# Performance work log

Hardware: AMD Instinct MI355X
Metric: run time of the kernel (lower is better)

Reference implementation:

```python
import jax, jax.numpy as jnp
import numpy as np
from jax import lax

BS, K, N = 8, 8, 16            # batch, gathers per sample, picks per curve
T, WG = 3072, 64               # gather time samples, traces
H, WC = 256, 256               # CVEncoder ScaleSize
RH, RW = 1024, 512             # resize (also GatherEncoder outLen=RH)
T0, T1 = 0.0, 7000.0           # tInt[0], tInt[-1]


def setup_inputs() -> dict:
    key = jax.random.key(0)
    ks = jax.random.split(key, 8)
    gather = jax.random.normal(ks[0], (BS, K, T, WG), jnp.float32)
    # cv: times sorted, strictly > 0, within [T0, T1]; velocities within VMM range
    times = jnp.sort(jax.random.uniform(ks[1], (BS, K, N), minval=100.0, maxval=T1), axis=-1)
    vels = jnp.sort(jax.random.uniform(ks[2], (BS, K, N), minval=1500.0, maxval=4500.0), axis=-1)
    cv = jnp.stack([times, vels], axis=-1).astype(jnp.float32)
    VMM = jnp.tile(jnp.array([1500.0, 4500.0], jnp.float32), (BS, 1))
    def cw(k, shape):
        return (jax.random.normal(k, shape, jnp.float32) * 0.1)
    params = dict(
        w1=cw(ks[3], (1, 1, 3, 3)), b1=jnp.zeros((1,), jnp.float32), g1=jnp.ones((1,), jnp.float32), be1=jnp.zeros((1,), jnp.float32),
        w2=cw(ks[4], (2, 3, 3, 3)), b2=jnp.zeros((2,), jnp.float32), g2=jnp.ones((2,), jnp.float32), be2=jnp.zeros((2,), jnp.float32),
        w3=cw(ks[5], (1, 2, 3, 2)), b3=jnp.zeros((1,), jnp.float32), g3=jnp.ones((1,), jnp.float32), be3=jnp.zeros((1,), jnp.float32),
        wf=cw(ks[6], (1, 1, 3, 3)), bf=jnp.zeros((1,), jnp.float32), gf=jnp.ones((1,), jnp.float32), bef=jnp.zeros((1,), jnp.float32),
    )
    return {"gather": gather, "cv": cv, "VMM": VMM, **params}


def _conv(x, w, b, stride, pad):
    y = lax.conv_general_dilated(x, w, stride, pad, dimension_numbers=("NCHW", "OIHW", "NCHW"))
    return y + b[None, :, None, None]


def _bn(x, g, b, eps=1e-5):
    # training-mode BatchNorm2d: stats over (N, H, W)
    m = jnp.mean(x, (0, 2, 3), keepdims=True)
    v = jnp.var(x, (0, 2, 3), keepdims=True)
    return (x - m) / jnp.sqrt(v + eps) * g[None, :, None, None] + b[None, :, None, None]


def _lrelu(x):
    return jnp.where(x >= 0, x, 0.1 * x)


def _cbl(x, w, b, g, be, stride):
    return _lrelu(_bn(_conv(x, w, b, stride, "VALID"), g, be))


def _maxpool(x, k):
    p = k // 2
    return lax.reduce_window(x, -jnp.inf, lax.max, (1, 1, k, k), (1, 1, 1, 1),
                             ((0, 0), (0, 0), (p, p), (p, p)))


def _cv_mask(cv, VMM):
    # normalize times to fractional row index and velocities to fractional col index
    dt = (T1 - T0) / (H - 1)
    t_idx = (cv[..., 0] - T0) / dt                                        # (BS,K,N)
    dv = (VMM[:, 1] - VMM[:, 0]) / (WC - 1)                               # (BS,)
    v_idx = (cv[..., 1] - VMM[:, 0, None, None]) / dv[:, None, None]      # (BS,K,N)
    t_flat = t_idx.reshape(-1, N)
    v_flat = v_idx.reshape(-1, N)
    tq = jnp.arange(H, dtype=jnp.float32)
    # per-curve piecewise-linear interpolation of v over the time grid
    v_curve = jax.vmap(lambda xp, fp: jnp.interp(tq, xp, fp))(t_flat, v_flat)  # (M,H)
    v_int = jnp.clip(v_curve.astype(jnp.int32), 0, WC - 1)
    M = BS * K
    mask = jnp.full((M, H, WC), 0.01, jnp.float32)
    mask = mask.at[jnp.arange(M)[:, None], jnp.arange(H)[None, :], v_int].add(0.9)
    mask = mask.reshape(BS, K, H, WC)
    # bilinear resize, half-pixel centers == torch align_corners=False
    return jax.image.resize(mask, (BS, K, RH, RW), method="linear")


def _forward(gather, cv, VMM, w1, b1, g1, be1, w2, b2, g2, be2, w3, b3, g3, be3, wf, bf, gf, bef):
    cv_mask = lax.stop_gradient(_cv_mask(cv, VMM))          # CVEncoder runs under no_grad
    x = gather.reshape(-1, 1, T, WG)                        # (BS*K,1,T,WG)
    x = x / jnp.max(jnp.abs(x))                             # mode='mute': keep sign
    x = _cbl(x, w1, b1, g1, be1, (3, 2))                    # (M,1,1024,31)
    xcat = jnp.concatenate([x, _maxpool(x, 3), _maxpool(x, 5)], axis=1)
    x = _cbl(xcat, w2, b2, g2, be2, (3, 2))                 # (M,2,341,15)
    x = _cbl(x, w3, b3, g3, be3, (3, 2))                    # (M,1,113,7)
    x = jax.image.resize(x, (x.shape[0], 1, RH, 1), method="linear")
    genr = x.reshape(BS, K, RH, 1)
    mix = jnp.sum(genr * cv_mask, axis=1, keepdims=True)    # (BS,1,RH,RW)
    y = _conv(mix, wf, bf, (1, 1), ((1, 1), (1, 1)))
    return _lrelu(_bn(y, gf, bef))


def reference(gather, cv, VMM, w1, b1, g1, be1, w2, b2, g2, be2, w3, b3, g3, be3, wf, bf, gf, bef):
    return _forward(gather, cv, VMM, w1, b1, g1, be1, w2, b2, g2, be2, w3, b3, g3, be3, wf, bf, gf, bef)
```

## Files before the change

### kernel.cpp

```cpp
#include <hip/hip_runtime.h>
#include <math.h>

#define BSZ 8
#define KG  8
#define NP  16
#define MM  64
#define TT  3072
#define WGN 64
#define HH  256
#define WCN 256
#define RHN 1024
#define RWN 512

#define C1H 1024
#define C1W 31
#define C2H 341
#define C2W 15
#define C3H 113
#define C3W 7

#define N1 (MM*C1H*C1W)
#define N2 (MM*C2H*C2W)
#define N3 (MM*C3H*C3W)
#define NF (BSZ*RHN*RWN)

#define SL 8

#define OFF_VINT 768
#define OFF_Y1   (OFF_VINT + MM*HH*4)
#define OFF_Y2   (OFF_Y1  + N1*4)
#define OFF_Y3   (OFF_Y2  + 2*N2*4)
#define OFF_GENR (OFF_Y3  + N3*4)

__device__ __forceinline__ void blockAdd2(double s, double ss, double* o0, double* o1) {
    __shared__ double red[4][2];
    __syncthreads();
    int lane = threadIdx.x & 63, wid = threadIdx.x >> 6;
#pragma unroll
    for (int off = 32; off > 0; off >>= 1) {
        s  += __shfl_down(s,  off, 64);
        ss += __shfl_down(ss, off, 64);
    }
    if (lane == 0) { red[wid][0] = s; red[wid][1] = ss; }
    __syncthreads();
    if (threadIdx.x == 0) {
        double a = 0, b = 0;
        int nw = blockDim.x >> 6;
        for (int i = 0; i < nw; i++) { a += red[i][0]; b += red[i][1]; }
        int slot = blockIdx.x & (SL - 1);
        atomicAdd(&o0[slot], a); atomicAdd(&o1[slot], b);
    }
}

__device__ __forceinline__ float2 bn_ab(const double* __restrict__ sums, int c,
                                        const float* __restrict__ g,
                                        const float* __restrict__ be, double n) {
    double sum = 0, sumsq = 0;
#pragma unroll
    for (int j = 0; j < SL; j++) {
        sum   += sums[(2 * c) * SL + j];
        sumsq += sums[(2 * c + 1) * SL + j];
    }
    double mean = sum / n;
    double var  = sumsq / n - mean * mean;
    double a = (double)g[c] / sqrt(var + 1e-5);
    return make_float2((float)a, (float)((double)be[c] - mean * a));
}

__global__ void k_conv1(const float* __restrict__ g, const float* __restrict__ w1,
                        const float* __restrict__ b1,
                        float* __restrict__ y1, double* sums) {
    float w[9];
#pragma unroll
    for (int i = 0; i < 9; i++) w[i] = w1[i];
    float bb = b1[0];
    double s = 0, ss = 0;
    int stride = gridDim.x * blockDim.x;
    for (int idx = blockIdx.x * blockDim.x + threadIdx.x; idx < N1; idx += stride) {
        int ow = idx % C1W;
        int t2 = idx / C1W;
        int oh = t2 % C1H;
        int m  = t2 / C1H;
        const float* xp = g + (size_t)m * TT * WGN + (size_t)(oh * 3) * WGN + ow * 2;
        float acc = bb;
#pragma unroll
        for (int r = 0; r < 3; r++)
#pragma unroll
            for (int c = 0; c < 3; c++) acc += w[r * 3 + c] * xp[r * WGN + c];
        y1[idx] = acc;
        s += acc; ss += (double)acc * (double)acc;
    }
    blockAdd2(s, ss, &sums[0], &sums[SL]);
}

#define F2_OH 32
#define F2_NCH 11
#define F2_NRMAX (3*F2_OH + 4)
__global__ void k_fused2(const float* __restrict__ y1, const double* __restrict__ sums_r,
                         const float* __restrict__ g1, const float* __restrict__ be1,
                         const float* __restrict__ w2, const float* __restrict__ b2,
                         float* __restrict__ y2, double* sums) {
    __shared__ float sact[F2_NRMAX][32];
    __shared__ float sr3[F2_NRMAX][32];
    __shared__ float sr5[F2_NRMAX][32];
    float2 ab1 = bn_ab(sums_r, 0, g1, be1, (double)N1);
    int m   = blockIdx.x / F2_NCH;
    int ch  = blockIdx.x % F2_NCH;
    int oh0 = ch * F2_OH;
    int OHa = min(F2_OH, C2H - oh0);
    int NR  = 3 * OHa + 4;
    int gl0 = 3 * oh0 - 2;
    const float* yp = y1 + (size_t)m * C1H * C1W;
    for (int i = threadIdx.x; i < NR * C1W; i += blockDim.x) {
        int l = i / C1W, w = i % C1W;
        int gr = gl0 + l;
        float v = -INFINITY;
        if (gr >= 0 && gr < C1H) {
            v = ab1.x * yp[gr * C1W + w] + ab1.y;
            v = v >= 0.f ? v : 0.1f * v;
        }
        sact[l][w] = v;
    }
    __syncthreads();
    for (int i = threadIdx.x; i < NR * C1W; i += blockDim.x) {
        int l = i / C1W, w = i % C1W;
        int wl1 = max(w - 1, 0), wr1 = min(w + 1, C1W - 1);
        int wl2 = max(w - 2, 0), wr2 = min(w + 2, C1W - 1);
        float c  = sact[l][w];
        float m3 = fmaxf(fmaxf(sact[l][wl1], c), sact[l][wr1]);
        float m5 = fmaxf(fmaxf(m3, sact[l][wl2]), sact[l][wr2]);
        sr3[l][w] = m3;
        sr5[l][w] = m5;
    }
    __syncthreads();
    double s0 = 0, ss0 = 0, s1 = 0, ss1 = 0;
    for (int o = threadIdx.x; o < OHa * C2W; o += blockDim.x) {
        int lo = o / C2W, ow = o % C2W;
        float a0 = b2[0], acc1 = b2[1];
#pragma unroll
        for (int i = 0; i < 3; i++) {
            int l = 3 * lo + 2 + i;
#pragma unroll
            for (int j = 0; j < 3; j++) {
                int wc = 2 * ow + j;
                float v0 = sact[l][wc];
                float v1 = fmaxf(fmaxf(sr3[l - 1][wc], sr3[l][wc]), sr3[l + 1][wc]);
                float v2 = fmaxf(fmaxf(fmaxf(sr5[l - 2][wc], sr5[l - 1][wc]), sr5[l][wc]),
                                 fmaxf(sr5[l + 1][wc], sr5[l + 2][wc]));
                int ki = i * 3 + j;
                a0   += w2[ki] * v0 + w2[9 + ki] * v1 + w2[18 + ki] * v2;
                acc1 += w2[27 + ki] * v0 + w2[36 + ki] * v1 + w2[45 + ki] * v2;
            }
        }
        size_t ob = (size_t)m * (2 * C2H * C2W) + (size_t)(oh0 + lo) * C2W + ow;
        y2[ob] = a0;
        y2[ob + C2H * C2W] = acc1;
        s0 += a0; ss0 += (double)a0 * a0;
        s1 += acc1; ss1 += (double)acc1 * acc1;
    }
    blockAdd2(s0, ss0, &sums[2 * SL], &sums[3 * SL]);
    blockAdd2(s1, ss1, &sums[4 * SL], &sums[5 * SL]);
}

__global__ void k_conv3(const float* __restrict__ y2, const double* __restrict__ sums_r,
                        const float* __restrict__ g2, const float* __restrict__ be2,
                        const float* __restrict__ w3, const float* __restrict__ b3,
                        float* __restrict__ y3, double* sums) {
    float2 ab20 = bn_ab(sums_r + 2 * SL, 0, g2, be2, (double)N2);
    float2 ab21 = bn_ab(sums_r + 2 * SL, 1, g2, be2, (double)N2);
    double s = 0, ss = 0;
    int stride = gridDim.x * blockDim.x;
    for (int idx = blockIdx.x * blockDim.x + threadIdx.x; idx < N3; idx += stride) {
        int ow = idx % C3W;
        int t2 = idx / C3W;
        int oh = t2 % C3H;
        int m  = t2 / C3H;
        float acc = b3[0];
#pragma unroll
        for (int i = 0; i < 2; i++) {
            float aa = i ? ab21.x : ab20.x, bb = i ? ab21.y : ab20.y;
            const float* cp = y2 + (size_t)m * (2 * C2H * C2W) + (size_t)i * C2H * C2W
                              + (size_t)(oh * 3) * C2W + ow * 2;
#pragma unroll
            for (int r = 0; r < 3; r++)
#pragma unroll
                for (int c = 0; c < 2; c++) {
                    float v = aa * cp[r * C2W + c] + bb;
                    v = v >= 0.f ? v : 0.1f * v;
                    acc += w3[i * 6 + r * 2 + c] * v;
                }
        }
        y3[idx] = acc;
        s += acc; ss += (double)acc * acc;
    }
    blockAdd2(s, ss, &sums[6 * SL], &sums[7 * SL]);
}

__global__ void k_vintgenr(const float* __restrict__ cv, const float* __restrict__ VMM,
                           const float* __restrict__ y3, const double* __restrict__ sums_r,
                           const float* __restrict__ g3, const float* __restrict__ be3,
                           int* __restrict__ vint, float* __restrict__ genr) {
    __shared__ float tt[NP], vv[NP];
    __shared__ float tile[C3H * C3W];
    int m = blockIdx.x;
    int b = m >> 3;
    float2 ab3 = bn_ab(sums_r + 6 * SL, 0, g3, be3, (double)N3);
    if (threadIdx.x < NP) {
        int n = threadIdx.x;
        float t = cv[(m * NP + n) * 2 + 0];
        float v = cv[(m * NP + n) * 2 + 1];
        float dt = 7000.0f / 255.0f;
        tt[n] = t / dt;
        float vmin = VMM[b * 2], vmax = VMM[b * 2 + 1];
        float dv = (vmax - vmin) / 255.0f;
        vv[n] = (v - vmin) / dv;
    }
    for (int i = threadIdx.x; i < C3H * C3W; i += blockDim.x) {
        float v = ab3.x * y3[m * C3H * C3W + i] + ab3.y;
        tile[i] = v >= 0.f ? v : 0.1f * v;
    }
    __syncthreads();
    {
        int h = threadIdx.x;
        float x = (float)h;
        float val;
        if (x <= tt[0]) val = vv[0];
        else if (x >= tt[NP - 1]) val = vv[NP - 1];
        else {
            int i = 1;
            while (i < NP - 1 && tt[i] <= x) i++;
            float d = tt[i] - tt[i - 1];
            val = (d != 0.f) ? vv[i - 1] + (x - tt[i - 1]) / d * (vv[i] - vv[i - 1]) : vv[i];
        }
        int vi = (int)val;
        vint[m * HH + h] = max(0, min(WCN - 1, vi));
    }
    const float cw0 = 4.f / 37.f, cw1 = 5.f / 37.f, cw2 = 6.f / 37.f, cw3 = 7.f / 37.f;
    const float cw[7] = { cw0, cw1, cw2, cw3, cw2, cw1, cw0 };
    for (int i = threadIdx.x; i < RHN; i += blockDim.x) {
        float sh = (i + 0.5f) * (113.0f / 1024.0f) - 0.5f;
        float fl = floorf(sh);
        float fr = sh - fl;
        int i0 = (int)fl, i1 = i0 + 1;
        i0 = max(0, min(C3H - 1, i0));
        i1 = max(0, min(C3H - 1, i1));
        float acc = 0.f;
#pragma unroll
        for (int x = 0; x < 7; x++) {
            float v = (1.f - fr) * tile[i0 * C3W + x] + fr * tile[i1 * C3W + x];
            acc += cw[x] * v;
        }
        genr[m * RHN + i] = acc;
    }
}

#define MC_TH 16
__device__ __forceinline__ void build_mix_tile(const float* __restrict__ genr,
                                               const int* __restrict__ vint,
                                               int b, int h0,
                                               float (*tile)[RWN + 2], float* Grow) {
    for (int i = threadIdx.x; i < (MC_TH + 2) * (RWN + 2); i += blockDim.x)
        ((float*)tile)[i] = 0.f;
    if (threadIdx.x < MC_TH + 2) Grow[threadIdx.x] = 0.f;
    __syncthreads();
    if (threadIdx.x < (MC_TH + 2) * KG) {
        int r = threadIdx.x / KG, k = threadIdx.x % KG;
        int h = h0 - 1 + r;
        if (h >= 0 && h < RHN) {
            int m = b * KG + k;
            float g = genr[m * RHN + h];
            atomicAdd(&Grow[r], g);
            float sh = (h + 0.5f) * 0.25f - 0.5f;
            float fl = floorf(sh);
            float fh = sh - fl;
            int ih0 = (int)fl, ih1 = ih0 + 1;
            ih0 = max(0, min(HH - 1, ih0));
            ih1 = max(0, min(HH - 1, ih1));
            int vv[2] = { vint[m * HH + ih0], vint[m * HH + ih1] };
            float aa[2] = { 0.9f * g * (1.f - fh), 0.9f * g * fh };
#pragma unroll
            for (int t = 0; t < 2; t++) {
                int v = vv[t]; float A = aa[t];
                if (v == 0) {
                    atomicAdd(&tile[r][1 + 0], A);
                    atomicAdd(&tile[r][1 + 1], 0.75f * A);
                    atomicAdd(&tile[r][1 + 2], 0.25f * A);
                } else if (v == WCN - 1) {
                    atomicAdd(&tile[r][1 + 509], 0.25f * A);
                    atomicAdd(&tile[r][1 + 510], 0.75f * A);
                    atomicAdd(&tile[r][1 + 511], A);
                } else {
                    atomicAdd(&tile[r][1 + 2 * v - 1], 0.25f * A);
                    atomicAdd(&tile[r][1 + 2 * v],     0.75f * A);
                    atomicAdd(&tile[r][1 + 2 * v + 1], 0.75f * A);
                    atomicAdd(&tile[r][1 + 2 * v + 2], 0.25f * A);
                }
            }
        }
    }
    __syncthreads();
    for (int i = threadIdx.x; i < (MC_TH + 2) * RWN; i += blockDim.x) {
        int r = i / RWN, w = i % RWN;
        int h = h0 - 1 + r;
        if (h >= 0 && h < RHN) tile[r][w + 1] += 0.01f * Grow[r];
    }
    __syncthreads();
}

__global__ void k_mixA(const float* __restrict__ genr, const int* __restrict__ vint,
                       const float* __restrict__ wf, const float* __restrict__ bf,
                       double* sums) {
    __shared__ float tile[MC_TH + 2][RWN + 2];
    __shared__ float Grow[MC_TH + 2];
    int b   = blockIdx.x / (RHN / MC_TH);
    int h0  = (blockIdx.x % (RHN / MC_TH)) * MC_TH;
    build_mix_tile(genr, vint, b, h0, tile, Grow);
    float w[9];
#pragma unroll
    for (int i = 0; i < 9; i++) w[i] = wf[i];
    float bb = bf[0];
    double s = 0, ss = 0;
    for (int o = threadIdx.x; o < MC_TH * RWN; o += blockDim.x) {
        int lr = o / RWN, x = o % RWN;
        float acc = bb;
#pragma unroll
        for (int dr = 0; dr < 3; dr++)
#pragma unroll
            for (int dc = 0; dc < 3; dc++)
                acc += w[dr * 3 + dc] * tile[lr + dr][x + dc];
        s += acc; ss += (double)acc * acc;
    }
    blockAdd2(s, ss, &sums[8 * SL], &sums[9 * SL]);
}

__global__ void k_mixB(const float* __restrict__ genr, const int* __restrict__ vint,
                       const float* __restrict__ wf, const float* __restrict__ bf,
                       const double* __restrict__ sums_r, const float* __restrict__ gf,
                       const float* __restrict__ bef, float* __restrict__ out) {
    __shared__ float tile[MC_TH + 2][RWN + 2];
    __shared__ float Grow[MC_TH + 2];
    float2 abf = bn_ab(sums_r + 8 * SL, 0, gf, bef, (double)NF);
    int b   = blockIdx.x / (RHN / MC_TH);
    int h0  = (blockIdx.x % (RHN / MC_TH)) * MC_TH;
    build_mix_tile(genr, vint, b, h0, tile, Grow);
    float w[9];
#pragma unroll
    for (int i = 0; i < 9; i++) w[i] = wf[i];
    float bb = bf[0];
    for (int o = threadIdx.x; o < MC_TH * RWN; o += blockDim.x) {
        int lr = o / RWN, x = o % RWN;
        float acc = bb;
#pragma unroll
        for (int dr = 0; dr < 3; dr++)
#pragma unroll
            for (int dc = 0; dc < 3; dc++)
                acc += w[dr * 3 + dc] * tile[lr + dr][x + dc];
        float v = abf.x * acc + abf.y;
        out[((size_t)b * RHN + (h0 + lr)) * RWN + x] = v >= 0.f ? v : 0.1f * v;
    }
}

extern "C" void kernel_launch(void* const* d_in, const int* in_sizes, int n_in,
                              void* d_out, int out_size, void* d_ws, size_t ws_size,
                              hipStream_t stream) {
    const float* gather = (const float*)d_in[0];
    const float* cv     = (const float*)d_in[1];
    const float* VMM    = (const float*)d_in[2];
    const float* w1 = (const float*)d_in[3];
    const float* b1 = (const float*)d_in[4];
    const float* g1 = (const float*)d_in[5];
    const float* be1 = (const float*)d_in[6];
    const float* w2 = (const float*)d_in[7];
    const float* b2 = (const float*)d_in[8];
    const float* g2 = (const float*)d_in[9];
    const float* be2 = (const float*)d_in[10];
    const float* w3 = (const float*)d_in[11];
    const float* b3 = (const float*)d_in[12];
    const float* g3 = (const float*)d_in[13];
    const float* be3 = (const float*)d_in[14];
    const float* wf = (const float*)d_in[15];
    const float* bf = (const float*)d_in[16];
    const float* gf = (const float*)d_in[17];
    const float* bef = (const float*)d_in[18];
    float* out = (float*)d_out;

    char* ws = (char*)d_ws;
    double* sums = (double*)ws;
    int*   vint  = (int*)(ws + OFF_VINT);
    float* y1    = (float*)(ws + OFF_Y1);
    float* y2    = (float*)(ws + OFF_Y2);
    float* y3    = (float*)(ws + OFF_Y3);
    float* genr  = (float*)(ws + OFF_GENR);

    hipMemsetAsync(d_ws, 0, 640, stream);

    k_conv1<<<512, 256, 0, stream>>>(gather, w1, b1, y1, sums);
    k_fused2<<<MM * F2_NCH, 256, 0, stream>>>(y1, sums, g1, be1, w2, b2, y2, sums);
    k_conv3<<<198, 256, 0, stream>>>(y2, sums, g2, be2, w3, b3, y3, sums);
    k_vintgenr<<<MM, 256, 0, stream>>>(cv, VMM, y3, sums, g3, be3, vint, genr);
    k_mixA<<<BSZ * (RHN / MC_TH), 256, 0, stream>>>(genr, vint, wf, bf, sums);
    k_mixB<<<BSZ * (RHN / MC_TH), 256, 0, stream>>>(genr, vint, wf, bf, sums, gf, bef, out);
}
```

Measured before the change: 195.3 us.

## Stage conv1 input in shared memory and materialize final conv output for BN pass

Conv1 now assigns each block a 16-row strip and cooperatively loads the needed gather rows into shared memory with float4 loads before computing. The final mix stage stores its conv output to a workspace buffer during the statistics pass. A simple vectorized BN+LeakyReLU kernel then replaces the second full tile rebuild and conv recompute. This trades extra global traffic (write and read of the full output-sized buffer) for removing a duplicated atomic-heavy tile construction, and it requires a larger workspace.

Result: slower. 227.0 us (+16.2%).

```diff
diff --git a/kernel.cpp b/kernel.cpp
--- a/kernel.cpp
+++ b/kernel.cpp
@@ -31,6 +31,7 @@
 #define OFF_Y2   (OFF_Y1  + N1*4)
 #define OFF_Y3   (OFF_Y2  + 2*N2*4)
 #define OFF_GENR (OFF_Y3  + N3*4)
+#define OFF_Y5   (OFF_GENR + MM*RHN*4)
 
 __device__ __forceinline__ void blockAdd2(double s, double ss, double* o0, double* o1) {
     __shared__ double red[4][2];
@@ -67,27 +68,36 @@
     return make_float2((float)a, (float)((double)be[c] - mean * a));
 }
 
+#define K1_R 16
+#define K1_ROWS (3*K1_R)
 __global__ void k_conv1(const float* __restrict__ g, const float* __restrict__ w1,
                         const float* __restrict__ b1,
                         float* __restrict__ y1, double* sums) {
+    __shared__ float sm[K1_ROWS * WGN];
+    int m   = blockIdx.x >> 6;
+    int ch  = blockIdx.x & 63;
+    int oh0 = ch * K1_R;
+    const float4* src = (const float4*)(g + (size_t)m * TT * WGN + (size_t)(oh0 * 3) * WGN);
+    float4* dst = (float4*)sm;
+#pragma unroll
+    for (int i = 0; i < 3; i++)
+        dst[threadIdx.x + i * 256] = src[threadIdx.x + i * 256];
     float w[9];
 #pragma unroll
     for (int i = 0; i < 9; i++) w[i] = w1[i];
     float bb = b1[0];
+    __syncthreads();
     double s = 0, ss = 0;
-    int stride = gridDim.x * blockDim.x;
-    for (int idx = blockIdx.x * blockDim.x + threadIdx.x; idx < N1; idx += stride) {
-        int ow = idx % C1W;
-        int t2 = idx / C1W;
-        int oh = t2 % C1H;
-        int m  = t2 / C1H;
-        const float* xp = g + (size_t)m * TT * WGN + (size_t)(oh * 3) * WGN + ow * 2;
+    float* yb = y1 + (size_t)m * C1H * C1W + (size_t)oh0 * C1W;
+    for (int o = threadIdx.x; o < K1_R * C1W; o += 256) {
+        int lo = o / C1W, ow = o % C1W;
+        const float* xp = sm + (3 * lo) * WGN + ow * 2;
         float acc = bb;
 #pragma unroll
         for (int r = 0; r < 3; r++)
 #pragma unroll
             for (int c = 0; c < 3; c++) acc += w[r * 3 + c] * xp[r * WGN + c];
-        y1[idx] = acc;
+        yb[o] = acc;
         s += acc; ss += (double)acc * (double)acc;
     }
     blockAdd2(s, ss, &sums[0], &sums[SL]);
@@ -309,7 +319,7 @@
 
 __global__ void k_mixA(const float* __restrict__ genr, const int* __restrict__ vint,
                        const float* __restrict__ wf, const float* __restrict__ bf,
-                       double* sums) {
+                       float* __restrict__ y5, double* sums) {
     __shared__ float tile[MC_TH + 2][RWN + 2];
     __shared__ float Grow[MC_TH + 2];
     int b   = blockIdx.x / (RHN / MC_TH);
@@ -328,35 +338,30 @@
 #pragma unroll
             for (int dc = 0; dc < 3; dc++)
                 acc += w[dr * 3 + dc] * tile[lr + dr][x + dc];
+        y5[((size_t)b * RHN + (h0 + lr)) * RWN + x] = acc;
         s += acc; ss += (double)acc * acc;
     }
     blockAdd2(s, ss, &sums[8 * SL], &sums[9 * SL]);
 }
 
-__global__ void k_mixB(const float* __restrict__ genr, const int* __restrict__ vint,
-                       const float* __restrict__ wf, const float* __restrict__ bf,
-                       const double* __restrict__ sums_r, const float* __restrict__ gf,
-                       const float* __restrict__ bef, float* __restrict__ out) {
-    __shared__ float tile[MC_TH + 2][RWN + 2];
-    __shared__ float Grow[MC_TH + 2];
+__global__ void k_bnf(const float* __restrict__ y5, const double* __restrict__ sums_r,
+                      const float* __restrict__ gf, const float* __restrict__ bef,
+                      float* __restrict__ out) {
     float2 abf = bn_ab(sums_r + 8 * SL, 0, gf, bef, (double)NF);
-    int b   = blockIdx.x / (RHN / MC_TH);
-    int h0  = (blockIdx.x % (RHN / MC_TH)) * MC_TH;
-    build_mix_tile(genr, vint, b, h0, tile, Grow);
-    float w[9];
-#pragma unroll
-    for (int i = 0; i < 9; i++) w[i] = wf[i];
-    float bb = bf[0];
-    for (int o = threadIdx.x; o < MC_TH * RWN; o += blockDim.x) {
-        int lr = o / RWN, x = o % RWN;
-        float acc = bb;
-#pragma unroll
-        for (int dr = 0; dr < 3; dr++)
-#pragma unroll
-            for (int dc = 0; dc < 3; dc++)
-                acc += w[dr * 3 + dc] * tile[lr + dr][x + dc];
-        float v = abf.x * acc + abf.y;
-        out[((size_t)b * RHN + (h0 + lr)) * RWN + x] = v >= 0.f ? v : 0.1f * v;
+    int stride = gridDim.x * blockDim.x;
+    const float4* src = (const float4*)y5;
+    float4* dst = (float4*)out;
+    for (int i = blockIdx.x * blockDim.x + threadIdx.x; i < NF / 4; i += stride) {
+        float4 v = src[i];
+        float a0 = abf.x * v.x + abf.y;
+        float a1 = abf.x * v.y + abf.y;
+        float a2 = abf.x * v.z + abf.y;
+        float a3 = abf.x * v.w + abf.y;
+        v.x = a0 >= 0.f ? a0 : 0.1f * a0;
+        v.y = a1 >= 0.f ? a1 : 0.1f * a1;
+        v.z = a2 >= 0.f ? a2 : 0.1f * a2;
+        v.w = a3 >= 0.f ? a3 : 0.1f * a3;
+        dst[i] = v;
     }
 }
 
@@ -391,13 +396,14 @@
     float* y2    = (float*)(ws + OFF_Y2);
     float* y3    = (float*)(ws + OFF_Y3);
     float* genr  = (float*)(ws + OFF_GENR);
+    float* y5    = (float*)(ws + OFF_Y5);
 
     hipMemsetAsync(d_ws, 0, 640, stream);
 
-    k_conv1<<<512, 256, 0, stream>>>(gather, w1, b1, y1, sums);
+    k_conv1<<<MM * (C1H / K1_R), 256, 0, stream>>>(gather, w1, b1, y1, sums);
     k_fused2<<<MM * F2_NCH, 256, 0, stream>>>(y1, sums, g1, be1, w2, b2, y2, sums);
     k_conv3<<<198, 256, 0, stream>>>(y2, sums, g2, be2, w3, b3, y3, sums);
     k_vintgenr<<<MM, 256, 0, stream>>>(cv, VMM, y3, sums, g3, be3, vint, genr);
-    k_mixA<<<BSZ * (RHN / MC_TH), 256, 0, stream>>>(genr, vint, wf, bf, sums);
-    k_mixB<<<BSZ * (RHN / MC_TH), 256, 0, stream>>>(genr, vint, wf, bf, sums, gf, bef, out);
-}
+    k_mixA<<<BSZ * (RHN / MC_TH), 256, 0, stream>>>(genr, vint, wf, bf, y5, sums);
+    k_bnf<<<2048, 256, 0, stream>>>(y5, sums, gf, bef, out);
+}
```
